# Kernel optimization log

Measured on AMD Instinct MI355X. Metric: run time of the kernel, lower is better.

The kernel has to match this reference:

```python
import jax, jax.numpy as jnp
import numpy as np

B, IN, D, L = 512, 512, 64, 256
WF = 0.5  # writter_f = 1.0 * w_0


def setup_inputs() -> dict:
    key = jax.random.key(0)
    ks = jax.random.split(key, 12)
    u = lambda i, s: jax.random.uniform(ks[i], s, jnp.float32, -0.05, 0.05)
    return {
        "x": jax.random.normal(ks[0], (B, IN), jnp.float32),
        "memory": u(1, (L, L)),
        "kernel_1": u(2, (IN, 60)), "bias_1": jnp.zeros((1, 60), jnp.float32),
        "kernel_2_0": u(3, (60, 50)), "bias_2_0": jnp.zeros((1, 50), jnp.float32),
        "kernel_3_0": u(4, (60, 50)), "bias_3_0": jnp.zeros((1, 50), jnp.float32),
        "kernel_4_0": u(5, (60, 50)), "bias_4_0": jnp.zeros((1, 50), jnp.float32),
        "kernel_2": u(6, (50, D)), "bias_2": jnp.zeros((1, D), jnp.float32),
        "kernel_3": u(7, (50, D)), "bias_3": jnp.zeros((1, D), jnp.float32),
        "kernel_4": u(8, (50, L)), "bias_4": jnp.zeros((1, L), jnp.float32),
        "kernel_r": u(9, (L, D, L)),
        "kernel_w": u(10, (L, D, L)),
        "w_sig": u(11, (L * L, 1)),
    }


def reference(x, memory, kernel_1, bias_1, kernel_2_0, bias_2_0, kernel_3_0,
              bias_3_0, kernel_4_0, bias_4_0, kernel_2, bias_2, kernel_3,
              bias_3, kernel_4, bias_4, kernel_r, kernel_w, w_sig):
    b = x.shape[0]
    l1 = jax.nn.relu(x @ kernel_1 + bias_1)                                  # (B, 60)
    # write path
    lfw = jax.nn.relu(jax.nn.relu(l1 @ kernel_3_0 + bias_3_0) @ kernel_3 + bias_3)  # (B, D)
    lbw = jnp.tanh(jax.nn.relu(l1 @ kernel_4_0 + bias_4_0) @ kernel_4 + bias_4)     # (B, L)
    lw = jax.nn.softmax(jnp.einsum('bd,jdl->jbl', lfw, kernel_w), axis=-1)   # (L, B, L)
    # wj = memory[j] * lwj * (1 + wf * lbw[j]); note lbw[j] indexes BATCH row j
    w = memory[:, None, :] * lw * (1.0 + WF * lbw[:L, None, :])              # (L, B, L)
    mem_new = w.reshape(L * b, L)                                            # concat over j on axis 0
    # read path (uses only first L rows of the updated memory)
    lf = jax.nn.relu(jax.nn.relu(l1 @ kernel_2_0 + bias_2_0) @ kernel_2 + bias_2)   # (B, D)
    lr = jax.nn.softmax(jnp.einsum('bd,idl->ibl', lf, kernel_r), axis=-1)    # (L, B, L)
    readed = (mem_new[:L][:, None, :] * lr).transpose(1, 0, 2).reshape(b, L * L)
    return jax.nn.sigmoid(readed @ w_sig)                                    # (B, 1)
```

## Files before the change

### kernel.cpp

```cpp
#include <hip/hip_runtime.h>
#include <hip/hip_bf16.h>
#include <math.h>


typedef __attribute__((ext_vector_type(8))) short short8;
typedef __attribute__((ext_vector_type(4))) float f32x4;

static __device__ __forceinline__ unsigned short f2bf(float f) {
    __hip_bfloat16 h = __float2bfloat16(f);
    return *reinterpret_cast<unsigned short*>(&h);
}

__global__ __launch_bounds__(256) void k_front(
    const float* __restrict__ x,
    const float* __restrict__ k1,  const float* __restrict__ b1,
    const float* __restrict__ k20, const float* __restrict__ b20,
    const float* __restrict__ k2,  const float* __restrict__ b2,
    const float* __restrict__ k30, const float* __restrict__ b30,
    const float* __restrict__ k3,  const float* __restrict__ b3,
    const float* __restrict__ k40, const float* __restrict__ b40,
    const float* __restrict__ k4,  const float* __restrict__ b4,
    unsigned short* __restrict__ lf_bf,
    float* __restrict__ lfw,
    float* __restrict__ lbw0) {
    __shared__ float xs[512];
    __shared__ float part[4][64];
    __shared__ float l1s[60];
    __shared__ float hid2[50], hid3[50], hid4[50];
    const int b = blockIdx.x, t = threadIdx.x;
    const int c = t & 63, kq = t >> 6;

    xs[t] = x[b * 512 + t];
    xs[t + 256] = x[b * 512 + 256 + t];
    __syncthreads();

    {
        float a = 0.f;
        if (c < 60) {
            const float* xk = xs + kq * 128;
            const float* kp = k1 + (kq * 128) * 60 + c;
#pragma unroll 8
            for (int k = 0; k < 128; ++k) a += xk[k] * kp[k * 60];
        }
        part[kq][c] = a;
    }
    __syncthreads();
    if (t < 60)
        l1s[t] = fmaxf(b1[t] + part[0][t] + part[1][t] + part[2][t] + part[3][t], 0.f);
    __syncthreads();

    if (t < 50) {
        float a = b20[t];
#pragma unroll
        for (int k = 0; k < 60; ++k) a += l1s[k] * k20[k * 50 + t];
        hid2[t] = fmaxf(a, 0.f);
    } else if (t >= 64 && t < 114 && b < 256) {
        const int j = t - 64;
        float a = b30[j];
#pragma unroll
        for (int k = 0; k < 60; ++k) a += l1s[k] * k30[k * 50 + j];
        hid3[j] = fmaxf(a, 0.f);
    } else if (t >= 128 && t < 178 && b == 0) {
        const int j = t - 128;
        float a = b40[j];
#pragma unroll
        for (int k = 0; k < 60; ++k) a += l1s[k] * k40[k * 50 + j];
        hid4[j] = fmaxf(a, 0.f);
    }
    __syncthreads();

    if (t < 64) {
        float a = b2[t];
#pragma unroll
        for (int k = 0; k < 50; ++k) a += hid2[k] * k2[k * 64 + t];
        lf_bf[b * 64 + t] = f2bf(fmaxf(a, 0.f));
    } else if (t < 128 && b < 256) {
        const int j = t - 64;
        float a = b3[j];
#pragma unroll
        for (int k = 0; k < 50; ++k) a += hid3[k] * k3[k * 64 + j];
        lfw[b * 64 + j] = fmaxf(a, 0.f);
    }
    if (b == 0) {
        __syncthreads();
        float a = b4[t];
#pragma unroll
        for (int k = 0; k < 50; ++k) a += hid4[k] * k4[k * 256 + t];
        lbw0[t] = tanhf(a);
    }
}

__global__ __launch_bounds__(512, 2) void k_mainc(
    const unsigned short* __restrict__ lf,
    const float* __restrict__ kernel_r,
    const float* __restrict__ lfw,
    const float* __restrict__ kw,
    const float* __restrict__ mem,
    const float* __restrict__ lbw0,
    const float* __restrict__ wsig,
    float* __restrict__ partial) {
    __shared__ __align__(16) unsigned short KrT[256 * 64];
    __shared__ float cLDS[256];
    __shared__ float wpart[4];
    const int i = blockIdx.x;
    const int tid = threadIdx.x;
    const int lane = tid & 63;
    const int wv = tid >> 6;

    {
        const int l = tid & 255;
        const int dh = tid >> 8;
        const int rot = ((l >> 3) & 15) * 2;
        const float* src = kernel_r + (size_t)i * 16384 + l;
        char* lds = (char*)KrT;
#pragma unroll
        for (int j = 0; j < 16; ++j) {
            const int d = dh * 32 + ((2 * j + rot) & 31);
            const float f0 = src[(size_t)d * 256];
            const float f1 = src[(size_t)(d + 1) * 256];
            const unsigned int pk =
                (unsigned int)f2bf(f0) | ((unsigned int)f2bf(f1) << 16);
            const int byteoff = ((l * 64 + d) * 2) ^ ((l & 7) << 4);
            *(unsigned int*)(lds + byteoff) = pk;
        }
    }

    float e_c = 0.f;
    if (tid < 256) {
        const int l = tid;
        float s = 0.f;
#pragma unroll 8
        for (int d = 0; d < 64; ++d) s += lfw[i * 64 + d] * kw[d * 256 + l];
        e_c = __expf(s);
        float se = e_c;
#pragma unroll
        for (int off = 1; off < 64; off <<= 1) se += __shfl_xor(se, off, 64);
        if (lane == 0) wpart[wv] = se;
    }
    __syncthreads();
    if (tid < 256) {
        const int l = tid;
        const float tot = wpart[0] + wpart[1] + wpart[2] + wpart[3];
        cLDS[l] = mem[l] * (e_c / tot) * (1.f + 0.5f * lbw0[l]) * wsig[i * 256 + l];
    }
    __syncthreads();

    const int c = lane & 15, g = lane >> 4;

    short8 Bf0[16], Bf1[16];
    {
        const char* lds = (const char*)KrT;
#pragma unroll
        for (int n = 0; n < 16; ++n) {
            const int l = n * 16 + c;
            const int base = l * 128 + g * 16;
            Bf0[n] = *(const short8*)(lds + ((base) ^ ((l & 7) << 4)));
            Bf1[n] = *(const short8*)(lds + ((base + 64) ^ ((l & 7) << 4)));
        }
    }
    float ccv[16];
#pragma unroll
    for (int n = 0; n < 16; ++n) ccv[n] = cLDS[n * 16 + c];

#pragma unroll
    for (int p = 0; p < 4; ++p) {
        const int b0 = wv * 64 + p * 16;
        const short8 a0 = *(const short8*)(lf + (b0 + c) * 64 + g * 8);
        const short8 a1 = *(const short8*)(lf + (b0 + c) * 64 + 32 + g * 8);
        f32x4 acc[16];
#pragma unroll
        for (int n = 0; n < 16; ++n) acc[n] = (f32x4){0.f, 0.f, 0.f, 0.f};
#pragma unroll
        for (int n = 0; n < 16; ++n) {
            acc[n] = __builtin_amdgcn_mfma_f32_16x16x32_bf16(a0, Bf0[n], acc[n], 0, 0, 0);
            acc[n] = __builtin_amdgcn_mfma_f32_16x16x32_bf16(a1, Bf1[n], acc[n], 0, 0, 0);
        }
#pragma unroll
        for (int r = 0; r < 4; ++r) {
            float se = 0.f, sw = 0.f;
#pragma unroll
            for (int n = 0; n < 16; ++n) {
                const float e = __expf(acc[n][r]);
                se += e;
                sw += ccv[n] * e;
            }
#pragma unroll
            for (int off = 1; off < 16; off <<= 1) {
                se += __shfl_xor(se, off, 64);
                sw += __shfl_xor(sw, off, 64);
            }
            if (c == 0) partial[(b0 + g * 4 + r) * 256 + i] = sw / se;
        }
    }
}

__global__ __launch_bounds__(256) void k_out2(const float* __restrict__ partial,
                                              float* __restrict__ out) {
    const int t = threadIdx.x;
    const int rq = t >> 6, lane = t & 63;
#pragma unroll
    for (int p = 0; p < 2; ++p) {
        const int row = blockIdx.x * 8 + p * 4 + rq;
        const f32x4 v = *(const f32x4*)&partial[row * 256 + lane * 4];
        float s = v.x + v.y + v.z + v.w;
#pragma unroll
        for (int off = 1; off < 64; off <<= 1) s += __shfl_xor(s, off, 64);
        if (lane == 0) out[row] = 1.f / (1.f + __expf(-s));
    }
}

extern "C" void kernel_launch(void* const* d_in, const int* in_sizes, int n_in,
                              void* d_out, int out_size, void* d_ws, size_t ws_size,
                              hipStream_t stream) {
    (void)in_sizes; (void)n_in; (void)out_size; (void)ws_size;
    const float* x    = (const float*)d_in[0];
    const float* mem  = (const float*)d_in[1];
    const float* k1   = (const float*)d_in[2];
    const float* b1   = (const float*)d_in[3];
    const float* k20  = (const float*)d_in[4];
    const float* b20  = (const float*)d_in[5];
    const float* k30  = (const float*)d_in[6];
    const float* b30  = (const float*)d_in[7];
    const float* k40  = (const float*)d_in[8];
    const float* b40  = (const float*)d_in[9];
    const float* k2   = (const float*)d_in[10];
    const float* b2   = (const float*)d_in[11];
    const float* k3   = (const float*)d_in[12];
    const float* b3   = (const float*)d_in[13];
    const float* k4   = (const float*)d_in[14];
    const float* b4   = (const float*)d_in[15];
    const float* kr   = (const float*)d_in[16];
    const float* kw   = (const float*)d_in[17];
    const float* wsig = (const float*)d_in[18];
    float* out = (float*)d_out;

    float* ws   = (float*)d_ws;
    float* lfw  = ws;
    float* lbw0 = lfw + 256 * 64;
    float* part = lbw0 + 256;
    unsigned short* lf_bf = (unsigned short*)(part + 131072);

    hipLaunchKernelGGL(k_front, dim3(512), dim3(256), 0, stream, x,
                       k1, b1, k20, b20, k2, b2, k30, b30, k3, b3,
                       k40, b40, k4, b4, lf_bf, lfw, lbw0);
    hipLaunchKernelGGL(k_mainc, dim3(256), dim3(512), 0, stream,
                       lf_bf, kr, lfw, kw, mem, lbw0, wsig, part);
    hipLaunchKernelGGL(k_out2,  dim3(64),  dim3(256), 0, stream, part, out);
}
```

Measured before the change: 32.67 us.

## Split softmax L dimension across two blocks per row and combine partial sums

The main kernel now launches two blocks per memory row i, each covering half of the 256-wide softmax axis. Each block writes an unnormalised (sum of exp, weighted sum) pair, and the output kernel merges the halves before the sigmoid. This doubles the grid, halves LDS and register use per block and raises the occupancy hint, so more of the GPU's compute units are busy. The cost is that the logit of the row is recomputed in both blocks (e_c softmax), the partial buffer grows fourfold, and the final reduction does more reads. The front kernel's first matmul also gets four independent accumulators to break the serial dependency chain.

New measurement: 32.70 us. No clear change (+0.1%).

```diff
diff --git a/kernel.cpp b/kernel.cpp
--- a/kernel.cpp
+++ b/kernel.cpp
@@ -5,6 +5,7 @@
 
 typedef __attribute__((ext_vector_type(8))) short short8;
 typedef __attribute__((ext_vector_type(4))) float f32x4;
+typedef __attribute__((ext_vector_type(2))) float f32x2;
 
 static __device__ __forceinline__ unsigned short f2bf(float f) {
     __hip_bfloat16 h = __float2bfloat16(f);
@@ -35,14 +36,19 @@
     __syncthreads();
 
     {
-        float a = 0.f;
+        float a0 = 0.f, a1 = 0.f, a2 = 0.f, a3 = 0.f;
         if (c < 60) {
             const float* xk = xs + kq * 128;
             const float* kp = k1 + (kq * 128) * 60 + c;
-#pragma unroll 8
-            for (int k = 0; k < 128; ++k) a += xk[k] * kp[k * 60];
-        }
-        part[kq][c] = a;
+#pragma unroll 4
+            for (int k = 0; k < 128; k += 4) {
+                a0 += xk[k + 0] * kp[(k + 0) * 60];
+                a1 += xk[k + 1] * kp[(k + 1) * 60];
+                a2 += xk[k + 2] * kp[(k + 2) * 60];
+                a3 += xk[k + 3] * kp[(k + 3) * 60];
+            }
+        }
+        part[kq][c] = (a0 + a1) + (a2 + a3);
     }
     __syncthreads();
     if (t < 60)
@@ -90,7 +96,7 @@
     }
 }
 
-__global__ __launch_bounds__(512, 2) void k_mainc(
+__global__ __launch_bounds__(512, 4) void k_mainc(
     const unsigned short* __restrict__ lf,
     const float* __restrict__ kernel_r,
     const float* __restrict__ lfw,
@@ -99,23 +105,24 @@
     const float* __restrict__ lbw0,
     const float* __restrict__ wsig,
     float* __restrict__ partial) {
-    __shared__ __align__(16) unsigned short KrT[256 * 64];
+    __shared__ __align__(16) unsigned short KrT[128 * 64];
     __shared__ float cLDS[256];
     __shared__ float wpart[4];
-    const int i = blockIdx.x;
+    const int i = blockIdx.x >> 1;
+    const int h = blockIdx.x & 1;
     const int tid = threadIdx.x;
     const int lane = tid & 63;
     const int wv = tid >> 6;
 
     {
-        const int l = tid & 255;
-        const int dh = tid >> 8;
-        const int rot = ((l >> 3) & 15) * 2;
-        const float* src = kernel_r + (size_t)i * 16384 + l;
+        const int l = tid & 127;
+        const int dh = tid >> 7;
+        const int rot = ((l >> 3) & 7) * 2;
+        const float* src = kernel_r + (size_t)i * 16384 + h * 128 + l;
         char* lds = (char*)KrT;
 #pragma unroll
-        for (int j = 0; j < 16; ++j) {
-            const int d = dh * 32 + ((2 * j + rot) & 31);
+        for (int j = 0; j < 8; ++j) {
+            const int d = dh * 16 + ((2 * j + rot) & 15);
             const float f0 = src[(size_t)d * 256];
             const float f1 = src[(size_t)(d + 1) * 256];
             const unsigned int pk =
@@ -147,31 +154,31 @@
 
     const int c = lane & 15, g = lane >> 4;
 
-    short8 Bf0[16], Bf1[16];
+    short8 Bf0[8], Bf1[8];
     {
         const char* lds = (const char*)KrT;
 #pragma unroll
-        for (int n = 0; n < 16; ++n) {
+        for (int n = 0; n < 8; ++n) {
             const int l = n * 16 + c;
             const int base = l * 128 + g * 16;
             Bf0[n] = *(const short8*)(lds + ((base) ^ ((l & 7) << 4)));
             Bf1[n] = *(const short8*)(lds + ((base + 64) ^ ((l & 7) << 4)));
         }
     }
-    float ccv[16];
-#pragma unroll
-    for (int n = 0; n < 16; ++n) ccv[n] = cLDS[n * 16 + c];
+    float ccv[8];
+#pragma unroll
+    for (int n = 0; n < 8; ++n) ccv[n] = cLDS[h * 128 + n * 16 + c];
 
 #pragma unroll
     for (int p = 0; p < 4; ++p) {
         const int b0 = wv * 64 + p * 16;
         const short8 a0 = *(const short8*)(lf + (b0 + c) * 64 + g * 8);
         const short8 a1 = *(const short8*)(lf + (b0 + c) * 64 + 32 + g * 8);
-        f32x4 acc[16];
-#pragma unroll
-        for (int n = 0; n < 16; ++n) acc[n] = (f32x4){0.f, 0.f, 0.f, 0.f};
-#pragma unroll
-        for (int n = 0; n < 16; ++n) {
+        f32x4 acc[8];
+#pragma unroll
+        for (int n = 0; n < 8; ++n) acc[n] = (f32x4){0.f, 0.f, 0.f, 0.f};
+#pragma unroll
+        for (int n = 0; n < 8; ++n) {
             acc[n] = __builtin_amdgcn_mfma_f32_16x16x32_bf16(a0, Bf0[n], acc[n], 0, 0, 0);
             acc[n] = __builtin_amdgcn_mfma_f32_16x16x32_bf16(a1, Bf1[n], acc[n], 0, 0, 0);
         }
@@ -179,7 +186,7 @@
         for (int r = 0; r < 4; ++r) {
             float se = 0.f, sw = 0.f;
 #pragma unroll
-            for (int n = 0; n < 16; ++n) {
+            for (int n = 0; n < 8; ++n) {
                 const float e = __expf(acc[n][r]);
                 se += e;
                 sw += ccv[n] * e;
@@ -189,7 +196,11 @@
                 se += __shfl_xor(se, off, 64);
                 sw += __shfl_xor(sw, off, 64);
             }
-            if (c == 0) partial[(b0 + g * 4 + r) * 256 + i] = sw / se;
+            if (c == 0) {
+                const int b = b0 + g * 4 + r;
+                *(f32x2*)&partial[((size_t)b * 256 + i) * 4 + h * 2] =
+                    (f32x2){se, sw};
+            }
         }
     }
 }
@@ -201,8 +212,13 @@
 #pragma unroll
     for (int p = 0; p < 2; ++p) {
         const int row = blockIdx.x * 8 + p * 4 + rq;
-        const f32x4 v = *(const f32x4*)&partial[row * 256 + lane * 4];
-        float s = v.x + v.y + v.z + v.w;
+        float s = 0.f;
+#pragma unroll
+        for (int q = 0; q < 4; ++q) {
+            const int i = q * 64 + lane;
+            const f32x4 v = *(const f32x4*)&partial[((size_t)row * 256 + i) * 4];
+            s += (v.y + v.w) / (v.x + v.z);
+        }
 #pragma unroll
         for (int off = 1; off < 64; off <<= 1) s += __shfl_xor(s, off, 64);
         if (lane == 0) out[row] = 1.f / (1.f + __expf(-s));
@@ -238,12 +254,12 @@
     float* lfw  = ws;
     float* lbw0 = lfw + 256 * 64;
     float* part = lbw0 + 256;
-    unsigned short* lf_bf = (unsigned short*)(part + 131072);
+    unsigned short* lf_bf = (unsigned short*)(part + 524288);
 
     hipLaunchKernelGGL(k_front, dim3(512), dim3(256), 0, stream, x,
                        k1, b1, k20, b20, k2, b2, k30, b30, k3, b3,
                        k40, b40, k4, b4, lf_bf, lfw, lbw0);
-    hipLaunchKernelGGL(k_mainc, dim3(256), dim3(512), 0, stream,
+    hipLaunchKernelGGL(k_mainc, dim3(512), dim3(512), 0, stream,
                        lf_bf, kr, lfw, kw, mem, lbw0, wsig, part);
     hipLaunchKernelGGL(k_out2,  dim3(64),  dim3(256), 0, stream, part, out);
 }
```

## Fuse final reduction into main kernel via atomics and last-block sigmoid

Applied to the files above, without the earlier changes.

Drops the third kernel launch and the 512x256 partial buffer. Each main-kernel block now atomically adds its per-row contributions into a 512-entry accumulator, and the last block to finish (found through an agent-scope counter) applies the sigmoid. The front kernel zeroes the accumulator and the counter, and its first matmul loop is split into four independent accumulators for more ILP. The cost is atomic contention on 512 addresses from 256 blocks and a result whose floating-point order is no longer deterministic.

Measured after the change: 59.94 us. 83.4% more time.

```diff
diff --git a/kernel.cpp b/kernel.cpp
--- a/kernel.cpp
+++ b/kernel.cpp
@@ -22,7 +22,9 @@
     const float* __restrict__ k4,  const float* __restrict__ b4,
     unsigned short* __restrict__ lf_bf,
     float* __restrict__ lfw,
-    float* __restrict__ lbw0) {
+    float* __restrict__ lbw0,
+    float* __restrict__ out_acc,
+    unsigned int* __restrict__ done) {
     __shared__ float xs[512];
     __shared__ float part[4][64];
     __shared__ float l1s[60];
@@ -30,19 +32,30 @@
     const int b = blockIdx.x, t = threadIdx.x;
     const int c = t & 63, kq = t >> 6;
 
+    if (b == 511) {
+        out_acc[t] = 0.f;
+        out_acc[t + 256] = 0.f;
+        if (t == 0) *done = 0u;
+    }
+
     xs[t] = x[b * 512 + t];
     xs[t + 256] = x[b * 512 + 256 + t];
     __syncthreads();
 
     {
-        float a = 0.f;
+        float a0 = 0.f, a1 = 0.f, a2 = 0.f, a3 = 0.f;
         if (c < 60) {
             const float* xk = xs + kq * 128;
             const float* kp = k1 + (kq * 128) * 60 + c;
-#pragma unroll 8
-            for (int k = 0; k < 128; ++k) a += xk[k] * kp[k * 60];
-        }
-        part[kq][c] = a;
+#pragma unroll 4
+            for (int k = 0; k < 128; k += 4) {
+                a0 += xk[k + 0] * kp[(k + 0) * 60];
+                a1 += xk[k + 1] * kp[(k + 1) * 60];
+                a2 += xk[k + 2] * kp[(k + 2) * 60];
+                a3 += xk[k + 3] * kp[(k + 3) * 60];
+            }
+        }
+        part[kq][c] = (a0 + a1) + (a2 + a3);
     }
     __syncthreads();
     if (t < 60)
@@ -98,10 +111,13 @@
     const float* __restrict__ mem,
     const float* __restrict__ lbw0,
     const float* __restrict__ wsig,
-    float* __restrict__ partial) {
+    float* __restrict__ out_acc,
+    unsigned int* __restrict__ done,
+    float* __restrict__ out) {
     __shared__ __align__(16) unsigned short KrT[256 * 64];
     __shared__ float cLDS[256];
     __shared__ float wpart[4];
+    __shared__ unsigned int lastflag;
     const int i = blockIdx.x;
     const int tid = threadIdx.x;
     const int lane = tid & 63;
@@ -189,23 +205,21 @@
                 se += __shfl_xor(se, off, 64);
                 sw += __shfl_xor(sw, off, 64);
             }
-            if (c == 0) partial[(b0 + g * 4 + r) * 256 + i] = sw / se;
-        }
-    }
-}
-
-__global__ __launch_bounds__(256) void k_out2(const float* __restrict__ partial,
-                                              float* __restrict__ out) {
-    const int t = threadIdx.x;
-    const int rq = t >> 6, lane = t & 63;
-#pragma unroll
-    for (int p = 0; p < 2; ++p) {
-        const int row = blockIdx.x * 8 + p * 4 + rq;
-        const f32x4 v = *(const f32x4*)&partial[row * 256 + lane * 4];
-        float s = v.x + v.y + v.z + v.w;
-#pragma unroll
-        for (int off = 1; off < 64; off <<= 1) s += __shfl_xor(s, off, 64);
-        if (lane == 0) out[row] = 1.f / (1.f + __expf(-s));
+            if (c == 0) atomicAdd(&out_acc[b0 + g * 4 + r], sw / se);
+        }
+    }
+
+    __syncthreads();
+    if (tid == 0) {
+        __threadfence();
+        lastflag = __hip_atomic_fetch_add(done, 1u, __ATOMIC_ACQ_REL,
+                                          __HIP_MEMORY_SCOPE_AGENT);
+    }
+    __syncthreads();
+    if (lastflag == 255u) {
+        const float v = __hip_atomic_load(&out_acc[tid], __ATOMIC_ACQUIRE,
+                                          __HIP_MEMORY_SCOPE_AGENT);
+        out[tid] = 1.f / (1.f + __expf(-v));
     }
 }
 
@@ -237,13 +251,13 @@
     float* ws   = (float*)d_ws;
     float* lfw  = ws;
     float* lbw0 = lfw + 256 * 64;
-    float* part = lbw0 + 256;
-    unsigned short* lf_bf = (unsigned short*)(part + 131072);
+    float* oacc = lbw0 + 256;
+    unsigned int* done = (unsigned int*)(oacc + 512);
+    unsigned short* lf_bf = (unsigned short*)(done + 64);
 
     hipLaunchKernelGGL(k_front, dim3(512), dim3(256), 0, stream, x,
                        k1, b1, k20, b20, k2, b2, k30, b30, k3, b3,
-                       k40, b40, k4, b4, lf_bf, lfw, lbw0);
+                       k40, b40, k4, b4, lf_bf, lfw, lbw0, oacc, done);
     hipLaunchKernelGGL(k_mainc, dim3(256), dim3(512), 0, stream,
-                       lf_bf, kr, lfw, kw, mem, lbw0, wsig, part);
-    hipLaunchKernelGGL(k_out2,  dim3(64),  dim3(256), 0, stream, part, out);
-}
+                       lf_bf, kr, lfw, kw, mem, lbw0, wsig, oacc, done, out);
+}
```

## Pre-convert kernel_r to padded bf16 layout in front kernel, DMA into LDS

Applied to the files above, without the earlier changes.

Adds 256 extra blocks to the front kernel that convert kernel_r from fp32 to bf16 and transpose it into a padded row layout (144-byte stride) in workspace. The main kernel then copies that buffer straight into LDS with global_load_lds and reads it without the XOR swizzle, since the padding avoids bank conflicts. The goal is to take the strided fp32 gathers and conversion off the main kernel's critical path and overlap them with the front MLP work. The cost is an extra bf16 round trip through global memory and a larger LDS footprint, which could reduce occupancy. The first-layer dot product is also split into four accumulators to shorten the dependency chain.

Result: no change. 33.07 us (+1.2%).

```diff
diff --git a/kernel.cpp b/kernel.cpp
--- a/kernel.cpp
+++ b/kernel.cpp
@@ -5,6 +5,10 @@
 
 typedef __attribute__((ext_vector_type(8))) short short8;
 typedef __attribute__((ext_vector_type(4))) float f32x4;
+typedef __attribute__((ext_vector_type(4))) unsigned int u32x4;
+
+#define KRT_STRIDE_B 144
+#define KRT_I_BYTES 40960
 
 static __device__ __forceinline__ unsigned short f2bf(float f) {
     __hip_bfloat16 h = __float2bfloat16(f);
@@ -20,14 +24,40 @@
     const float* __restrict__ k3,  const float* __restrict__ b3,
     const float* __restrict__ k40, const float* __restrict__ b40,
     const float* __restrict__ k4,  const float* __restrict__ b4,
+    const float* __restrict__ kernel_r,
     unsigned short* __restrict__ lf_bf,
     float* __restrict__ lfw,
-    float* __restrict__ lbw0) {
+    float* __restrict__ lbw0,
+    unsigned short* __restrict__ krt) {
+    const int blk = blockIdx.x, t = threadIdx.x;
+
+    if (blk >= 512) {
+        const int i = blk - 512;
+        const float* src = kernel_r + (size_t)i * 16384 + t;
+        unsigned short* dst = krt + (size_t)i * (KRT_I_BYTES / 2)
+                                  + (size_t)t * (KRT_STRIDE_B / 2);
+#pragma unroll
+        for (int ch = 0; ch < 4; ++ch) {
+            unsigned int pk[8];
+#pragma unroll
+            for (int j = 0; j < 8; ++j) {
+                const float f0 = src[(size_t)(ch * 16 + 2 * j) * 256];
+                const float f1 = src[(size_t)(ch * 16 + 2 * j + 1) * 256];
+                pk[j] = (unsigned int)f2bf(f0) | ((unsigned int)f2bf(f1) << 16);
+            }
+            u32x4 w0 = (u32x4){pk[0], pk[1], pk[2], pk[3]};
+            u32x4 w1 = (u32x4){pk[4], pk[5], pk[6], pk[7]};
+            *(u32x4*)(dst + ch * 16) = w0;
+            *(u32x4*)(dst + ch * 16 + 8) = w1;
+        }
+        return;
+    }
+
     __shared__ float xs[512];
     __shared__ float part[4][64];
     __shared__ float l1s[60];
     __shared__ float hid2[50], hid3[50], hid4[50];
-    const int b = blockIdx.x, t = threadIdx.x;
+    const int b = blk;
     const int c = t & 63, kq = t >> 6;
 
     xs[t] = x[b * 512 + t];
@@ -35,14 +65,19 @@
     __syncthreads();
 
     {
-        float a = 0.f;
+        float a0 = 0.f, a1 = 0.f, a2 = 0.f, a3 = 0.f;
         if (c < 60) {
             const float* xk = xs + kq * 128;
             const float* kp = k1 + (kq * 128) * 60 + c;
-#pragma unroll 8
-            for (int k = 0; k < 128; ++k) a += xk[k] * kp[k * 60];
-        }
-        part[kq][c] = a;
+#pragma unroll 4
+            for (int k = 0; k < 128; k += 4) {
+                a0 += xk[k + 0] * kp[(k + 0) * 60];
+                a1 += xk[k + 1] * kp[(k + 1) * 60];
+                a2 += xk[k + 2] * kp[(k + 2) * 60];
+                a3 += xk[k + 3] * kp[(k + 3) * 60];
+            }
+        }
+        part[kq][c] = (a0 + a1) + (a2 + a3);
     }
     __syncthreads();
     if (t < 60)
@@ -92,14 +127,14 @@
 
 __global__ __launch_bounds__(512, 2) void k_mainc(
     const unsigned short* __restrict__ lf,
-    const float* __restrict__ kernel_r,
+    const unsigned short* __restrict__ krt,
     const float* __restrict__ lfw,
     const float* __restrict__ kw,
     const float* __restrict__ mem,
     const float* __restrict__ lbw0,
     const float* __restrict__ wsig,
     float* __restrict__ partial) {
-    __shared__ __align__(16) unsigned short KrT[256 * 64];
+    __shared__ __align__(16) unsigned char KrT[KRT_I_BYTES];
     __shared__ float cLDS[256];
     __shared__ float wpart[4];
     const int i = blockIdx.x;
@@ -108,20 +143,15 @@
     const int wv = tid >> 6;
 
     {
-        const int l = tid & 255;
-        const int dh = tid >> 8;
-        const int rot = ((l >> 3) & 15) * 2;
-        const float* src = kernel_r + (size_t)i * 16384 + l;
-        char* lds = (char*)KrT;
-#pragma unroll
-        for (int j = 0; j < 16; ++j) {
-            const int d = dh * 32 + ((2 * j + rot) & 31);
-            const float f0 = src[(size_t)d * 256];
-            const float f1 = src[(size_t)(d + 1) * 256];
-            const unsigned int pk =
-                (unsigned int)f2bf(f0) | ((unsigned int)f2bf(f1) << 16);
-            const int byteoff = ((l * 64 + d) * 2) ^ ((l & 7) << 4);
-            *(unsigned int*)(lds + byteoff) = pk;
+        const char* gsrc = (const char*)krt + (size_t)i * KRT_I_BYTES
+                           + (size_t)(wv * 5) * 1024 + (lane << 4);
+        char* lds = (char*)KrT + (size_t)(wv * 5) * 1024;
+#pragma unroll
+        for (int k = 0; k < 5; ++k) {
+            __builtin_amdgcn_global_load_lds(
+                (const __attribute__((address_space(1))) void*)(gsrc + k * 1024),
+                (__attribute__((address_space(3))) void*)(lds + k * 1024),
+                16, 0, 0);
         }
     }
 
@@ -153,9 +183,9 @@
 #pragma unroll
         for (int n = 0; n < 16; ++n) {
             const int l = n * 16 + c;
-            const int base = l * 128 + g * 16;
-            Bf0[n] = *(const short8*)(lds + ((base) ^ ((l & 7) << 4)));
-            Bf1[n] = *(const short8*)(lds + ((base + 64) ^ ((l & 7) << 4)));
+            const char* row = lds + l * KRT_STRIDE_B + g * 16;
+            Bf0[n] = *(const short8*)(row);
+            Bf1[n] = *(const short8*)(row + 64);
         }
     }
     float ccv[16];
@@ -239,11 +269,12 @@
     float* lbw0 = lfw + 256 * 64;
     float* part = lbw0 + 256;
     unsigned short* lf_bf = (unsigned short*)(part + 131072);
-
-    hipLaunchKernelGGL(k_front, dim3(512), dim3(256), 0, stream, x,
+    unsigned short* krt   = lf_bf + 512 * 64;
+
+    hipLaunchKernelGGL(k_front, dim3(768), dim3(256), 0, stream, x,
                        k1, b1, k20, b20, k2, b2, k30, b30, k3, b3,
-                       k40, b40, k4, b4, lf_bf, lfw, lbw0);
+                       k40, b40, k4, b4, kr, lf_bf, lfw, lbw0, krt);
     hipLaunchKernelGGL(k_mainc, dim3(256), dim3(512), 0, stream,
-                       lf_bf, kr, lfw, kw, mem, lbw0, wsig, part);
+                       lf_bf, krt, lfw, kw, mem, lbw0, wsig, part);
     hipLaunchKernelGGL(k_out2,  dim3(64),  dim3(256), 0, stream, part, out);
 }
```
